# Performance work log

Hardware: AMD Instinct MI355X
Metric: run time of the kernel (lower is better)

Reference implementation:

```python
import jax, jax.numpy as jnp
import numpy as np

N, E, D_IN, D_H, D_OUT = 50000, 800000, 128, 128, 64


def _glorot(key, shape):
    fan_in, fan_out = shape[1], shape[0]
    lim = (6.0 / (fan_in + fan_out)) ** 0.5
    return jax.random.uniform(key, shape, jnp.float32, -lim, lim)


def setup_inputs() -> dict:
    key = jax.random.key(0)
    ks = jax.random.split(key, 8)
    x = jax.random.normal(ks[0], (N, D_IN), jnp.float32)
    edge_index = jax.random.randint(ks[1], (2, E), 0, N, jnp.int64)
    # SAGEConv layer 1: lin_l (on aggregated neighbors, with bias) and lin_r (root, no bias)
    W1l = _glorot(ks[2], (D_H, D_IN))
    b1 = jnp.zeros((D_H,), jnp.float32)
    W1r = _glorot(ks[3], (D_H, D_IN))
    # SAGEConv layer 2
    W2l = _glorot(ks[4], (D_OUT, D_H))
    b2 = jnp.zeros((D_OUT,), jnp.float32)
    W2r = _glorot(ks[5], (D_OUT, D_H))
    return {"x": x, "edge_index": edge_index, "W1l": W1l, "b1": b1, "W1r": W1r,
            "W2l": W2l, "b2": b2, "W2r": W2r}


def _sage_conv(x, src, dst, inv_deg, Wl, b, Wr):
    # mean-aggregate neighbor features: gather x[src], scatter-sum into dst, divide by degree
    msg_sum = jax.ops.segment_sum(x[src], dst, num_segments=N)  # [N, d]
    agg = msg_sum * inv_deg[:, None]
    return agg @ Wl.T + b + x @ Wr.T


def reference(x, edge_index, W1l, b1, W1r, W2l, b2, W2r):
    src, dst = edge_index[0], edge_index[1]
    deg = jax.ops.segment_sum(jnp.ones((E,), jnp.float32), dst, num_segments=N)
    inv_deg = jnp.where(deg > 0, 1.0 / jnp.maximum(deg, 1.0), 0.0)
    h = _sage_conv(x, src, dst, inv_deg, W1l, b1, W1r)
    h = jax.nn.relu(h)  # dropout is identity in eval mode
    out = _sage_conv(h, src, dst, inv_deg, W2l, b2, W2r)
    return out
```

## Files before the change

### kernel.cpp

```cpp
#include <hip/hip_runtime.h>
#include <hip/hip_bf16.h>

typedef __hip_bfloat16 bf16;
typedef __attribute__((ext_vector_type(8))) short short8;
typedef __attribute__((ext_vector_type(4))) float f32x4;
typedef unsigned short u16;

#define N_NODES 50000
#define NE      800000
#define DIN     128
#define DH      128
#define DOUT    64
#define MTILES  (N_NODES / 16)
#define CAP     64
#define DSTRIDE 8
#define NXCD    8
#define NPX     (N_NODES / NXCD)
#define ECHUNK  2048
#define NCHUNK  ((NE + ECHUNK - 1) / ECHUNK)
#define SCAT_BLKS (NCHUNK * NXCD)

__device__ __forceinline__ int clamp_node(int s) {
    return min(max(s, 0), N_NODES - 1);
}
__device__ __forceinline__ float b2f(short s) {
    unsigned u = ((unsigned)(unsigned short)s) << 16;
    float f; __builtin_memcpy(&f, &u, 4); return f;
}
__device__ __forceinline__ short f2b(float f) {
    __hip_bfloat16 h = __float2bfloat16(f);
    short s; __builtin_memcpy(&s, &h, 2); return s;
}

__global__ void k_build(const int* __restrict__ src, const int* __restrict__ dst,
                        int* __restrict__ degPad, u16* __restrict__ csrPad,
                        const float* __restrict__ x, __hip_bfloat162* __restrict__ xb2,
                        const float* __restrict__ W1l, const float* __restrict__ W1r,
                        const float* __restrict__ W2l, const float* __restrict__ W2r,
                        bf16* __restrict__ W1b, bf16* __restrict__ W2b) {
    int b = blockIdx.x;
    if (b < SCAT_BLKS) {
        int chunk = b >> 3;
        int lo = (b & 7) * NPX, hi = lo + NPX;
        int e0 = chunk * ECHUNK + threadIdx.x * 8;
        if (e0 + 7 < NE) {
            int4 d0 = *(const int4*)(dst + e0);
            int4 d1 = *(const int4*)(dst + e0 + 4);
            int4 s0 = *(const int4*)(src + e0);
            int4 s1 = *(const int4*)(src + e0 + 4);
            int dv[8] = {d0.x, d0.y, d0.z, d0.w, d1.x, d1.y, d1.z, d1.w};
            int sv[8] = {s0.x, s0.y, s0.z, s0.w, s1.x, s1.y, s1.z, s1.w};
            #pragma unroll
            for (int j = 0; j < 8; ++j) {
                int t = dv[j];
                if (t >= lo && t < hi) {
                    int pos = atomicAdd(&degPad[t * DSTRIDE], 1);
                    if (pos < CAP) csrPad[t * CAP + pos] = (u16)sv[j];
                }
            }
        }
    } else if (b < SCAT_BLKS + 6250) {
        int i = (b - SCAT_BLKS) * 256 + threadIdx.x;
        float4 v = ((const float4*)x)[i];
        __hip_bfloat162 a, bb;
        a.x = __float2bfloat16(v.x); a.y = __float2bfloat16(v.y);
        bb.x = __float2bfloat16(v.z); bb.y = __float2bfloat16(v.w);
        xb2[2 * i]     = a;
        xb2[2 * i + 1] = bb;
    } else {
        int i = (b - SCAT_BLKS - 6250) * 256 + threadIdx.x;
        if (i < 128 * 256) {
            int n = i >> 8, k = i & 255;
            float v = (k < 128) ? W1l[n * 128 + k] : W1r[n * 128 + (k - 128)];
            W1b[i] = __float2bfloat16(v);
        } else {
            int j = i - 128 * 256;
            int n = j >> 7, k = j & 127;
            float v = (n < 64) ? W2l[n * 128 + k] : W2r[(n - 64) * 128 + k];
            W2b[j] = __float2bfloat16(v);
        }
    }
}

__global__ __launch_bounds__(256) void k_fused1(const int* __restrict__ degPad,
                                                const u16* __restrict__ csrPad,
                                                const short* __restrict__ xb,
                                                const short* __restrict__ W1b,
                                                const float* __restrict__ b1,
                                                const short* __restrict__ W2b,
                                                bf16* __restrict__ pb,
                                                float* __restrict__ qbuf) {
    __shared__ short ms[16][136];
    __shared__ short hs[16][136];
    int wave = threadIdx.x >> 6, lane = threadIdx.x & 63;
    int q = lane >> 4, mr = lane & 15;
    int g = q, c = mr;
    int mt = blockIdx.x;
    #pragma unroll
    for (int it = 0; it < 4; ++it) {
        int row = wave * 4 + it;
        int node = mt * 16 + row;
        int d = min(max(degPad[node * DSTRIDE], 0), CAP);
        const u16* crow = csrPad + node * CAP;
        int idx[8];
        #pragma unroll
        for (int t = 0; t < 8; ++t) idx[t] = crow[t * 4 + g];
        float acc[8];
        #pragma unroll
        for (int j = 0; j < 8; ++j) acc[j] = 0.f;
        short8 v[8];
        #pragma unroll
        for (int t = 0; t < 8; ++t) {
            if (4 * t < d) {
                int n = clamp_node(idx[t]);
                v[t] = *(const short8*)(xb + (size_t)n * DIN + c * 8);
            }
        }
        #pragma unroll
        for (int t = 0; t < 8; ++t) {
            if (4 * t < d) {
                if (4 * t + g < d) {
                    #pragma unroll
                    for (int j = 0; j < 8; ++j) acc[j] += b2f(v[t][j]);
                }
            }
        }
        if (d > 32) {
            int idxh[8];
            #pragma unroll
            for (int t = 8; t < 16; ++t) idxh[t - 8] = crow[t * 4 + g];
            short8 vh[8];
            #pragma unroll
            for (int t = 8; t < 16; ++t) {
                if (4 * t < d) {
                    int n = clamp_node(idxh[t - 8]);
                    vh[t - 8] = *(const short8*)(xb + (size_t)n * DIN + c * 8);
                }
            }
            #pragma unroll
            for (int t = 8; t < 16; ++t) {
                if (4 * t < d) {
                    if (4 * t + g < d) {
                        #pragma unroll
                        for (int j = 0; j < 8; ++j) acc[j] += b2f(vh[t - 8][j]);
                    }
                }
            }
        }
        #pragma unroll
        for (int j = 0; j < 8; ++j) {
            acc[j] += __shfl_xor(acc[j], 16);
            acc[j] += __shfl_xor(acc[j], 32);
        }
        if (g == 0) {
            float inv = (d > 0) ? 1.0f / (float)d : 0.0f;
            short8 o;
            #pragma unroll
            for (int j = 0; j < 8; ++j) o[j] = f2b(acc[j] * inv);
            *(short8*)(&ms[row][c * 8]) = o;
        }
    }
    int n0 = wave * 32;
    short8 Bf1[2][8];
    #pragma unroll
    for (int t = 0; t < 2; ++t) {
        const short* wrow = W1b + (size_t)(n0 + t * 16 + mr) * 256 + q * 8;
        #pragma unroll
        for (int ks = 0; ks < 8; ++ks) Bf1[t][ks] = *(const short8*)(wrow + ks * 32);
    }
    float bias0 = b1[n0 + mr], bias1 = b1[n0 + 16 + mr];
    const short* a1 = xb + (size_t)(mt * 16 + mr) * DIN + q * 8;
    short8 Af[8];
    #pragma unroll
    for (int ks = 0; ks < 4; ++ks) Af[4 + ks] = *(const short8*)(a1 + ks * 32);
    __syncthreads();
    #pragma unroll
    for (int ks = 0; ks < 4; ++ks) Af[ks] = *(const short8*)(&ms[mr][ks * 32 + q * 8]);
    f32x4 acc0 = {0.f, 0.f, 0.f, 0.f}, acc1 = {0.f, 0.f, 0.f, 0.f};
    #pragma unroll
    for (int ks = 0; ks < 8; ++ks) {
        acc0 = __builtin_amdgcn_mfma_f32_16x16x32_bf16(Af[ks], Bf1[0][ks], acc0, 0, 0, 0);
        acc1 = __builtin_amdgcn_mfma_f32_16x16x32_bf16(Af[ks], Bf1[1][ks], acc1, 0, 0, 0);
    }
    short8 Bf2[2][4];
    #pragma unroll
    for (int t = 0; t < 2; ++t) {
        const short* wrow = W2b + (size_t)(n0 + t * 16 + mr) * 128 + q * 8;
        #pragma unroll
        for (int ks = 0; ks < 4; ++ks) Bf2[t][ks] = *(const short8*)(wrow + ks * 32);
    }
    #pragma unroll
    for (int r = 0; r < 4; ++r) {
        int row = q * 4 + r;
        float v0 = acc0[r] + bias0;
        float v1 = acc1[r] + bias1;
        hs[row][n0 + mr]      = f2b(v0 > 0.f ? v0 : 0.f);
        hs[row][n0 + 16 + mr] = f2b(v1 > 0.f ? v1 : 0.f);
    }
    __syncthreads();
    short8 Ah[4];
    #pragma unroll
    for (int ks = 0; ks < 4; ++ks) Ah[ks] = *(const short8*)(&hs[mr][ks * 32 + q * 8]);
    f32x4 c20 = {0.f, 0.f, 0.f, 0.f}, c21 = {0.f, 0.f, 0.f, 0.f};
    #pragma unroll
    for (int ks = 0; ks < 4; ++ks) {
        c20 = __builtin_amdgcn_mfma_f32_16x16x32_bf16(Ah[ks], Bf2[0][ks], c20, 0, 0, 0);
        c21 = __builtin_amdgcn_mfma_f32_16x16x32_bf16(Ah[ks], Bf2[1][ks], c21, 0, 0, 0);
    }
    #pragma unroll
    for (int r = 0; r < 4; ++r) {
        int row = mt * 16 + q * 4 + r;
        int c0 = n0 + mr, c1 = n0 + 16 + mr;
        if (c0 < 64) {
            pb[(size_t)row * 64 + c0] = __float2bfloat16(c20[r]);
            pb[(size_t)row * 64 + c1] = __float2bfloat16(c21[r]);
        } else {
            qbuf[(size_t)row * 64 + (c0 - 64)] = c20[r];
            qbuf[(size_t)row * 64 + (c1 - 64)] = c21[r];
        }
    }
}

__global__ __launch_bounds__(256) void k_agg2f(const int* __restrict__ degPad, const u16* __restrict__ csrPad,
                                               const short* __restrict__ pb, const float* __restrict__ qbuf,
                                               const float* __restrict__ b2, float* __restrict__ out) {
    int node = blockIdx.x * 4 + (threadIdx.x >> 6);
    if (node >= N_NODES) return;
    int lane = threadIdx.x & 63;
    int g = lane >> 3, c = lane & 7;
    int d = min(max(degPad[node * DSTRIDE], 0), CAP);
    const u16* crow = csrPad + node * CAP;
    int idx[4];
    #pragma unroll
    for (int t = 0; t < 4; ++t) idx[t] = crow[t * 8 + g];
    float acc[8];
    #pragma unroll
    for (int j = 0; j < 8; ++j) acc[j] = 0.f;
    short8 v[4];
    #pragma unroll
    for (int t = 0; t < 4; ++t) {
        if (8 * t < d) {
            int n = clamp_node(idx[t]);
            v[t] = *(const short8*)(pb + (size_t)n * 64 + c * 8);
        }
    }
    #pragma unroll
    for (int t = 0; t < 4; ++t) {
        if (8 * t < d) {
            if (8 * t + g < d) {
                #pragma unroll
                for (int j = 0; j < 8; ++j) acc[j] += b2f(v[t][j]);
            }
        }
    }
    if (d > 32) {
        int idxh[4];
        #pragma unroll
        for (int t = 4; t < 8; ++t) idxh[t - 4] = crow[t * 8 + g];
        short8 vh[4];
        #pragma unroll
        for (int t = 4; t < 8; ++t) {
            if (8 * t < d) {
                int n = clamp_node(idxh[t - 4]);
                vh[t - 4] = *(const short8*)(pb + (size_t)n * 64 + c * 8);
            }
        }
        #pragma unroll
        for (int t = 4; t < 8; ++t) {
            if (8 * t < d) {
                if (8 * t + g < d) {
                    #pragma unroll
                    for (int j = 0; j < 8; ++j) acc[j] += b2f(vh[t - 4][j]);
                }
            }
        }
    }
    #pragma unroll
    for (int j = 0; j < 8; ++j) {
        acc[j] += __shfl_xor(acc[j], 8);
        acc[j] += __shfl_xor(acc[j], 16);
        acc[j] += __shfl_xor(acc[j], 32);
    }
    if (g == 0) {
        float inv = (d > 0) ? 1.0f / (float)d : 0.0f;
        const float* qr = qbuf + (size_t)node * 64 + c * 8;
        const float* br = b2 + c * 8;
        float* orow = out + (size_t)node * 64 + c * 8;
        float4 o0, o1;
        o0.x = acc[0] * inv + qr[0] + br[0];
        o0.y = acc[1] * inv + qr[1] + br[1];
        o0.z = acc[2] * inv + qr[2] + br[2];
        o0.w = acc[3] * inv + qr[3] + br[3];
        o1.x = acc[4] * inv + qr[4] + br[4];
        o1.y = acc[5] * inv + qr[5] + br[5];
        o1.z = acc[6] * inv + qr[6] + br[6];
        o1.w = acc[7] * inv + qr[7] + br[7];
        ((float4*)orow)[0] = o0;
        ((float4*)orow)[1] = o1;
    }
}

extern "C" void kernel_launch(void* const* d_in, const int* in_sizes, int n_in,
                              void* d_out, int out_size, void* d_ws, size_t ws_size,
                              hipStream_t stream) {
    const float* x   = (const float*)d_in[0];
    const int*   ei  = (const int*)  d_in[1];
    const float* W1l = (const float*)d_in[2];
    const float* b1  = (const float*)d_in[3];
    const float* W1r = (const float*)d_in[4];
    const float* W2l = (const float*)d_in[5];
    const float* b2  = (const float*)d_in[6];
    const float* W2r = (const float*)d_in[7];
    float* out = (float*)d_out;

    const int* src = ei;
    const int* dst = ei + NE;

    char* ws = (char*)d_ws;
    int*   degPad = (int*)  (ws + 0);
    u16*   csrPad = (u16*)  (ws + 1600000);
    short* xb     = (short*)(ws + 8000000);
    bf16*  pb     = (bf16*) (ws + 20800000);
    float* qbuf   = (float*)(ws + 27200000);
    bf16*  W1b    = (bf16*) (ws + 40000000);
    bf16*  W2b    = (bf16*) (ws + 40065536);

    hipMemsetAsync(degPad, 0, 1600000, stream);

    k_build<<<SCAT_BLKS + 6250 + 192, 256, 0, stream>>>(src, dst, degPad, csrPad,
                                                        x, (__hip_bfloat162*)xb,
                                                        W1l, W1r, W2l, W2r, W1b, W2b);
    k_fused1<<<MTILES, 256, 0, stream>>>(degPad, csrPad, xb, (const short*)W1b, b1,
                                         (const short*)W2b, pb, qbuf);
    k_agg2f<<<(N_NODES + 3) / 4, 256, 0, stream>>>(degPad, csrPad, (const short*)pb, qbuf, b2, out);
}
```

Baseline: 212.9 us.

## Use 16 waves per tile in fused layer-1 kernel with wave-specialized GEMMs

Result: slower. 230.6 us (+8.3%).

```diff
diff --git a/kernel.cpp b/kernel.cpp
--- a/kernel.cpp
+++ b/kernel.cpp
@@ -82,23 +82,22 @@
     }
 }
 
-__global__ __launch_bounds__(256) void k_fused1(const int* __restrict__ degPad,
-                                                const u16* __restrict__ csrPad,
-                                                const short* __restrict__ xb,
-                                                const short* __restrict__ W1b,
-                                                const float* __restrict__ b1,
-                                                const short* __restrict__ W2b,
-                                                bf16* __restrict__ pb,
-                                                float* __restrict__ qbuf) {
+__global__ __launch_bounds__(1024) void k_fused1(const int* __restrict__ degPad,
+                                                 const u16* __restrict__ csrPad,
+                                                 const short* __restrict__ xb,
+                                                 const short* __restrict__ W1b,
+                                                 const float* __restrict__ b1,
+                                                 const short* __restrict__ W2b,
+                                                 bf16* __restrict__ pb,
+                                                 float* __restrict__ qbuf) {
     __shared__ short ms[16][136];
     __shared__ short hs[16][136];
     int wave = threadIdx.x >> 6, lane = threadIdx.x & 63;
     int q = lane >> 4, mr = lane & 15;
     int g = q, c = mr;
     int mt = blockIdx.x;
-    #pragma unroll
-    for (int it = 0; it < 4; ++it) {
-        int row = wave * 4 + it;
+    {
+        int row = wave;
         int node = mt * 16 + row;
         int d = min(max(degPad[node * DSTRIDE], 0), CAP);
         const u16* crow = csrPad + node * CAP;
@@ -160,63 +159,54 @@
             *(short8*)(&ms[row][c * 8]) = o;
         }
     }
-    int n0 = wave * 32;
-    short8 Bf1[2][8];
-    #pragma unroll
-    for (int t = 0; t < 2; ++t) {
-        const short* wrow = W1b + (size_t)(n0 + t * 16 + mr) * 256 + q * 8;
-        #pragma unroll
-        for (int ks = 0; ks < 8; ++ks) Bf1[t][ks] = *(const short8*)(wrow + ks * 32);
-    }
-    float bias0 = b1[n0 + mr], bias1 = b1[n0 + 16 + mr];
-    const short* a1 = xb + (size_t)(mt * 16 + mr) * DIN + q * 8;
-    short8 Af[8];
-    #pragma unroll
-    for (int ks = 0; ks < 4; ++ks) Af[4 + ks] = *(const short8*)(a1 + ks * 32);
+    int n0 = (wave & 7) * 16;
+    short8 Bf1[8], Af[8], Bf2[4];
+    float bias0 = 0.f;
+    if (wave < 8) {
+        const short* wrow = W1b + (size_t)(n0 + mr) * 256 + q * 8;
+        #pragma unroll
+        for (int ks = 0; ks < 8; ++ks) Bf1[ks] = *(const short8*)(wrow + ks * 32);
+        bias0 = b1[n0 + mr];
+        const short* a1 = xb + (size_t)(mt * 16 + mr) * DIN + q * 8;
+        #pragma unroll
+        for (int ks = 0; ks < 4; ++ks) Af[4 + ks] = *(const short8*)(a1 + ks * 32);
+    } else {
+        const short* wrow = W2b + (size_t)(n0 + mr) * 128 + q * 8;
+        #pragma unroll
+        for (int ks = 0; ks < 4; ++ks) Bf2[ks] = *(const short8*)(wrow + ks * 32);
+    }
     __syncthreads();
-    #pragma unroll
-    for (int ks = 0; ks < 4; ++ks) Af[ks] = *(const short8*)(&ms[mr][ks * 32 + q * 8]);
-    f32x4 acc0 = {0.f, 0.f, 0.f, 0.f}, acc1 = {0.f, 0.f, 0.f, 0.f};
-    #pragma unroll
-    for (int ks = 0; ks < 8; ++ks) {
-        acc0 = __builtin_amdgcn_mfma_f32_16x16x32_bf16(Af[ks], Bf1[0][ks], acc0, 0, 0, 0);
-        acc1 = __builtin_amdgcn_mfma_f32_16x16x32_bf16(Af[ks], Bf1[1][ks], acc1, 0, 0, 0);
-    }
-    short8 Bf2[2][4];
-    #pragma unroll
-    for (int t = 0; t < 2; ++t) {
-        const short* wrow = W2b + (size_t)(n0 + t * 16 + mr) * 128 + q * 8;
-        #pragma unroll
-        for (int ks = 0; ks < 4; ++ks) Bf2[t][ks] = *(const short8*)(wrow + ks * 32);
-    }
-    #pragma unroll
-    for (int r = 0; r < 4; ++r) {
-        int row = q * 4 + r;
-        float v0 = acc0[r] + bias0;
-        float v1 = acc1[r] + bias1;
-        hs[row][n0 + mr]      = f2b(v0 > 0.f ? v0 : 0.f);
-        hs[row][n0 + 16 + mr] = f2b(v1 > 0.f ? v1 : 0.f);
+    if (wave < 8) {
+        #pragma unroll
+        for (int ks = 0; ks < 4; ++ks) Af[ks] = *(const short8*)(&ms[mr][ks * 32 + q * 8]);
+        f32x4 acc0 = {0.f, 0.f, 0.f, 0.f};
+        #pragma unroll
+        for (int ks = 0; ks < 8; ++ks)
+            acc0 = __builtin_amdgcn_mfma_f32_16x16x32_bf16(Af[ks], Bf1[ks], acc0, 0, 0, 0);
+        #pragma unroll
+        for (int r = 0; r < 4; ++r) {
+            float v0 = acc0[r] + bias0;
+            hs[q * 4 + r][n0 + mr] = f2b(v0 > 0.f ? v0 : 0.f);
+        }
     }
     __syncthreads();
-    short8 Ah[4];
-    #pragma unroll
-    for (int ks = 0; ks < 4; ++ks) Ah[ks] = *(const short8*)(&hs[mr][ks * 32 + q * 8]);
-    f32x4 c20 = {0.f, 0.f, 0.f, 0.f}, c21 = {0.f, 0.f, 0.f, 0.f};
-    #pragma unroll
-    for (int ks = 0; ks < 4; ++ks) {
-        c20 = __builtin_amdgcn_mfma_f32_16x16x32_bf16(Ah[ks], Bf2[0][ks], c20, 0, 0, 0);
-        c21 = __builtin_amdgcn_mfma_f32_16x16x32_bf16(Ah[ks], Bf2[1][ks], c21, 0, 0, 0);
-    }
-    #pragma unroll
-    for (int r = 0; r < 4; ++r) {
-        int row = mt * 16 + q * 4 + r;
-        int c0 = n0 + mr, c1 = n0 + 16 + mr;
-        if (c0 < 64) {
-            pb[(size_t)row * 64 + c0] = __float2bfloat16(c20[r]);
-            pb[(size_t)row * 64 + c1] = __float2bfloat16(c21[r]);
-        } else {
-            qbuf[(size_t)row * 64 + (c0 - 64)] = c20[r];
-            qbuf[(size_t)row * 64 + (c1 - 64)] = c21[r];
+    if (wave >= 8) {
+        short8 Ah[4];
+        #pragma unroll
+        for (int ks = 0; ks < 4; ++ks) Ah[ks] = *(const short8*)(&hs[mr][ks * 32 + q * 8]);
+        f32x4 c20 = {0.f, 0.f, 0.f, 0.f};
+        #pragma unroll
+        for (int ks = 0; ks < 4; ++ks)
+            c20 = __builtin_amdgcn_mfma_f32_16x16x32_bf16(Ah[ks], Bf2[ks], c20, 0, 0, 0);
+        #pragma unroll
+        for (int r = 0; r < 4; ++r) {
+            int row = mt * 16 + q * 4 + r;
+            int c0 = n0 + mr;
+            if (n0 < 64) {
+                pb[(size_t)row * 64 + c0] = __float2bfloat16(c20[r]);
+            } else {
+                qbuf[(size_t)row * 64 + (c0 - 64)] = c20[r];
+            }
         }
     }
 }
@@ -330,7 +320,7 @@
     k_build<<<SCAT_BLKS + 6250 + 192, 256, 0, stream>>>(src, dst, degPad, csrPad,
                                                         x, (__hip_bfloat162*)xb,
                                                         W1l, W1r, W2l, W2r, W1b, W2b);
-    k_fused1<<<MTILES, 256, 0, stream>>>(degPad, csrPad, xb, (const short*)W1b, b1,
-                                         (const short*)W2b, pb, qbuf);
+    k_fused1<<<MTILES, 1024, 0, stream>>>(degPad, csrPad, xb, (const short*)W1b, b1,
+                                          (const short*)W2b, pb, qbuf);
     k_agg2f<<<(N_NODES + 3) / 4, 256, 0, stream>>>(degPad, csrPad, (const short*)pb, qbuf, b2, out);
 }
```
